# Kernel tuning notes

Measured on AMD Instinct MI355X. Metric: run time of the kernel, lower is better.

Reference implementation:

```python
import jax, jax.numpy as jnp
import numpy as np

B, C, H, W = 4, 3, 32, 32
N_IMAGES = 32
TIMESTEPS = 20


def _extract_patches(x, pad_mode):
    """3x3 patches at every spatial location. x: [B,C,H,W] -> [B,C,9,H,W]."""
    if pad_mode == 'wrap':
        xp = jnp.pad(x, ((0, 0), (0, 0), (1, 1), (1, 1)), mode='wrap')
    else:
        xp = jnp.pad(x, ((0, 0), (0, 0), (1, 1), (1, 1)))
    h, w = x.shape[2], x.shape[3]
    sl = [xp[:, :, di:di + h, dj:dj + w] for di in range(3) for dj in range(3)]
    return jnp.stack(sl, axis=2)  # [B,C,9,H,W], k = di*3+dj (torch unfold order)


def setup_inputs() -> dict:
    key = jax.random.key(0)
    k1, k2 = jax.random.split(key)
    x = jax.random.normal(k1, (B, C, H, W), dtype=jnp.float32)
    images = jax.random.uniform(k2, (N_IMAGES, C, H, W), dtype=jnp.float32)
    # linear beta schedule, as in _noise_buffers
    betas = jnp.linspace(1e-4, 0.02, TIMESTEPS, dtype=jnp.float32)
    alpha_cumprod = jnp.cumprod(1.0 - betas)
    mu_sched = jnp.sqrt(alpha_cumprod)
    sigma_sched = jnp.sqrt(1.0 - alpha_cumprod)
    return {"x": x, "images": images, "mu_sched": mu_sched,
            "sigma_sched": sigma_sched, "t": 10}


def reference(x, images, mu_sched, sigma_sched, t):
    mu = mu_sched[t]
    sigma = sigma_sched[t]
    b, c, h, w = x.shape

    # x-side: circular-padded 3x3 patches and their squared norms
    xp = _extract_patches(x, 'wrap').reshape(b, c * 9, h, w)   # [B,C*9,H,W]
    x_norms = jnp.sum(xp * xp, axis=1)                          # [B,H,W]

    # dataset-side: zero-padded 3x3 patches at every pixel of every image
    ip = _extract_patches(images, 'zeros')                      # [N,C,9,H,W]
    patches = ip.transpose(0, 3, 4, 1, 2).reshape(-1, c * 9)    # [P, C*9], P=N*H*W
    pnorms = jnp.sum(patches * patches, axis=1)                 # [P]
    pcenters = patches.reshape(-1, c, 9)[:, :, 4]               # [P,C] center pixel (1,1)

    # conv2d(x_pad, patches) == contraction over the C*9 patch axis
    conv = jnp.einsum('bkhw,pk->bphw', xp, patches)             # [B,P,H,W]

    inv2s2 = 1.0 / (2.0 * sigma * sigma)
    log_w = -(x_norms[:, None] - 2.0 * mu * conv
              + (mu * mu) * pnorms[None, :, None, None]) * inv2s2  # [B,P,H,W]

    # stable softmax-style weights over the patch axis (== online LSE result)
    m = jnp.max(log_w, axis=1)                                  # [B,H,W]
    wgt = jnp.exp(log_w - m[:, None])                           # [B,P,H,W]
    sum_w = jnp.sum(wgt, axis=1)                                # [B,H,W]

    # sum_p w * (x - mu * pcenter) = x*sum_w - mu * (w @ pcenters)
    wc = jnp.einsum('bphw,pc->bchw', wgt, pcenters)             # [B,C,H,W]
    sum_wd = x * sum_w[:, None] - mu * wc
    return -sum_wd / (sigma * sigma * sum_w[:, None])
```

## Files before the change

kernel.cpp:

```cpp
#include <hip/hip_runtime.h>
#include <cstddef>

#define P_TOTAL 32768
#define Q_TOTAL 4096
#define NSPLIT 128
#define KPS 256
#define TILES 16
#define NGROUP 8
#define QPERWG 256
#define NQG (Q_TOTAL / QPERWG)
#define GRID (NSPLIT * NQG)

#define KEYS_B 16384
#define VT_OFF KEYS_B
#define VT_PITCH 528
#define LDS_TOTAL (VT_OFF + 4 * VT_PITCH)

typedef _Float16 half8 __attribute__((ext_vector_type(8)));
typedef __fp16 fp16x2 __attribute__((ext_vector_type(2)));
typedef __fp16 fp16x4 __attribute__((ext_vector_type(4)));
typedef __fp16 fp16x8 __attribute__((ext_vector_type(8)));
typedef float floatx4 __attribute__((ext_vector_type(4)));

union h8cast { fp16x8 a; half8 b; };

__device__ __forceinline__ float fexp2(float x) {
#if defined(__has_builtin) && __has_builtin(__builtin_amdgcn_exp2f)
    return __builtin_amdgcn_exp2f(x);
#else
    return exp2f(x);
#endif
}

__global__ __launch_bounds__(256) void qbuild_k(
    const float* __restrict__ x, _Float16* __restrict__ q16)
{
    int q = blockIdx.x * 256 + threadIdx.x;
    int b = q >> 10, rem = q & 1023, h = rem >> 5, w = rem & 31;
    const float* xb = x + (size_t)b * 3072;
    _Float16 row[32];
    #pragma unroll
    for (int c = 0; c < 3; c++)
      #pragma unroll
      for (int di = 0; di < 3; di++)
        #pragma unroll
        for (int dj = 0; dj < 3; dj++)
            row[c * 9 + di * 3 + dj] =
                (_Float16)xb[c * 1024 + ((h + di + 31) & 31) * 32 + ((w + dj + 31) & 31)];
    row[27] = (_Float16)1.0f;
    row[28] = (_Float16)0.f; row[29] = (_Float16)0.f;
    row[30] = (_Float16)0.f; row[31] = (_Float16)0.f;
    _Float16* qp = q16 + (size_t)q * 32;
    #pragma unroll
    for (int u = 0; u < 4; u++) ((float4*)qp)[u] = ((float4*)row)[u];
}

__global__ __launch_bounds__(256) void score_k(
    const _Float16* __restrict__ q16, const float* __restrict__ images,
    const float* __restrict__ mu_sched, const float* __restrict__ sigma_sched,
    const int* __restrict__ tptr, float* __restrict__ partials)
{
    __shared__ char lds[LDS_TOTAL];
    int tid = threadIdx.x;
    int split = blockIdx.x >> 4;
    int qg    = blockIdx.x & 15;

    int t = tptr[0];
    float mu = mu_sched[t], sg = sigma_sched[t];
    const float LOG2E = 1.4426950408889634f;
    float inv2s2 = 1.0f / (2.0f * sg * sg);
    float s1     = 2.0f * mu * inv2s2 * LOG2E;
    float bscale = -mu * mu * inv2s2 * LOG2E;

    {
        int r = tid;
        int m16 = r & 15, tt = (r >> 4) & 1, tp = r >> 5;
        int kk = tp * 32 + (m16 >> 2) * 8 + tt * 4 + (m16 & 3);
        int p = split * KPS + kk;
        int n = p >> 10, rem = p & 1023, i = rem >> 5, j = rem & 31;
        const float* img = images + (size_t)n * 3072;
        _Float16 hrow[32];
        float pnorm = 0.f, c0 = 0.f, c1 = 0.f, c2 = 0.f;
        #pragma unroll
        for (int c = 0; c < 3; c++)
          #pragma unroll
          for (int di = 0; di < 3; di++)
            #pragma unroll
            for (int dj = 0; dj < 3; dj++) {
                int ii = i + di - 1, jj = j + dj - 1;
                float val = 0.f;
                if (ii >= 0 && ii < 32 && jj >= 0 && jj < 32)
                    val = img[c * 1024 + ii * 32 + jj];
                hrow[c * 9 + di * 3 + dj] = (_Float16)(val * s1);
                pnorm = fmaf(val, val, pnorm);
                if (di == 1 && dj == 1) { if (c == 0) c0 = val; else if (c == 1) c1 = val; else c2 = val; }
            }
        hrow[27] = (_Float16)(pnorm * bscale);
        hrow[28] = (_Float16)0.f; hrow[29] = (_Float16)0.f;
        hrow[30] = (_Float16)0.f; hrow[31] = (_Float16)0.f;
        int sw = (r >> 1) & 3;
        float4* src4 = (float4*)hrow;
        #pragma unroll
        for (int c = 0; c < 4; c++)
            *(float4*)(lds + r * 64 + ((c ^ sw) << 4)) = src4[c];
        _Float16* vt = (_Float16*)(lds + VT_OFF);
        vt[0 * (VT_PITCH / 2) + kk] = (_Float16)1.0f;
        vt[1 * (VT_PITCH / 2) + kk] = (_Float16)c0;
        vt[2 * (VT_PITCH / 2) + kk] = (_Float16)c1;
        vt[3 * (VT_PITCH / 2) + kk] = (_Float16)c2;
    }

    int lane = tid & 63, wid = tid >> 6;
    int col  = lane & 15, quad = lane >> 4;
    int qbase = qg * QPERWG + wid * 64;

    half8 qf[4];
    #pragma unroll
    for (int f = 0; f < 4; f++)
        qf[f] = *(const half8*)(q16 + (size_t)(qbase + f * 16 + col) * 32 + quad * 8);
    __syncthreads();

    int swc = (col >> 1) & 3;
    const char* abase = lds + col * 64 + ((quad ^ swc) << 4);

    float mx[4];
    {
        floatx4 mv[4];
        #pragma unroll
        for (int f = 0; f < 4; f++) mv[f] = (floatx4){-3e38f, -3e38f, -3e38f, -3e38f};
        #pragma unroll 4
        for (int tile = 0; tile < TILES; tile++) {
            half8 ak = *(const half8*)(abase + tile * 1024);
            #pragma unroll
            for (int f = 0; f < 4; f++) {
                floatx4 a = __builtin_amdgcn_mfma_f32_16x16x32_f16(
                    ak, qf[f], (floatx4){0.f, 0.f, 0.f, 0.f}, 0, 0, 0);
                mv[f] = __builtin_elementwise_max(mv[f], a);
            }
        }
        #pragma unroll
        for (int f = 0; f < 4; f++) {
            mx[f] = fmaxf(fmaxf(mv[f][0], mv[f][1]), fmaxf(mv[f][2], mv[f][3]));
            mx[f] = fmaxf(mx[f], __shfl_xor(mx[f], 16, 64));
            mx[f] = fmaxf(mx[f], __shfl_xor(mx[f], 32, 64));
        }
    }
    floatx4 nmv[4];
    #pragma unroll
    for (int f = 0; f < 4; f++)
        nmv[f] = (floatx4){-mx[f], -mx[f], -mx[f], -mx[f]};

    if (quad == 0) {
        #pragma unroll
        for (int f = 0; f < 4; f++)
            partials[(size_t)split * Q_TOTAL + qbase + f * 16 + col] = mx[f];
    }

    const char* vrow = lds + VT_OFF + col * VT_PITCH;
    floatx4 acc[4];
    #pragma unroll
    for (int f = 0; f < 4; f++) acc[f] = (floatx4){0.f, 0.f, 0.f, 0.f};

    #pragma unroll 2
    for (int g = 0; g < NGROUP; g++) {
        half8 ak0 = *(const half8*)(abase + (2 * g) * 1024);
        half8 ak1 = *(const half8*)(abase + (2 * g + 1) * 1024);
        half8 av = (half8)(_Float16)0.f;
        if (col < 4) av = *(const half8*)(vrow + g * 64 + quad * 16);
        #pragma unroll
        for (int f = 0; f < 4; f++) {
            floatx4 a0 = __builtin_amdgcn_mfma_f32_16x16x32_f16(ak0, qf[f], nmv[f], 0, 0, 0);
            floatx4 a1 = __builtin_amdgcn_mfma_f32_16x16x32_f16(ak1, qf[f], nmv[f], 0, 0, 0);
            fp16x2 p00 = __builtin_amdgcn_cvt_pkrtz(fexp2(a0[0]), fexp2(a0[1]));
            fp16x2 p01 = __builtin_amdgcn_cvt_pkrtz(fexp2(a0[2]), fexp2(a0[3]));
            fp16x2 p10 = __builtin_amdgcn_cvt_pkrtz(fexp2(a1[0]), fexp2(a1[1]));
            fp16x2 p11 = __builtin_amdgcn_cvt_pkrtz(fexp2(a1[2]), fexp2(a1[3]));
            fp16x4 lo = __builtin_shufflevector(p00, p01, 0, 1, 2, 3);
            fp16x4 hi = __builtin_shufflevector(p10, p11, 0, 1, 2, 3);
            h8cast u; u.a = __builtin_shufflevector(lo, hi, 0, 1, 2, 3, 4, 5, 6, 7);
            acc[f] = __builtin_amdgcn_mfma_f32_16x16x32_f16(av, u.b, acc[f], 0, 0, 0);
        }
    }

    if (quad == 0) {
        const size_t PL = (size_t)NSPLIT * Q_TOTAL;
        #pragma unroll
        for (int f = 0; f < 4; f++) {
            size_t idx = (size_t)split * Q_TOTAL + qbase + f * 16 + col;
            partials[idx + PL]     = acc[f][0];
            partials[idx + PL * 2] = acc[f][1];
            partials[idx + PL * 3] = acc[f][2];
            partials[idx + PL * 4] = acc[f][3];
        }
    }
}

__global__ __launch_bounds__(256) void combine_k(
    const float* __restrict__ x, const float* __restrict__ partials,
    const float* __restrict__ mu_sched, const float* __restrict__ sigma_sched,
    const int* __restrict__ tptr, float* __restrict__ out)
{
    int q = blockIdx.x * 256 + threadIdx.x;
    int t = tptr[0];
    float mu = mu_sched[t], sg = sigma_sched[t];
    float inv_s2 = 1.0f / (sg * sg);

    const size_t PL = (size_t)NSPLIT * Q_TOTAL;
    float M1 = -3e38f, S1 = 0.f, A1 = 0.f, B1 = 0.f, C1 = 0.f;
    float M2 = -3e38f, S2 = 0.f, A2 = 0.f, B2 = 0.f, C2 = 0.f;
    #pragma unroll 4
    for (int sp = 0; sp < NSPLIT / 2; sp++) {
        {
            size_t idx = (size_t)sp * Q_TOTAL + q;
            float mval = partials[idx];
            float mnew = fmaxf(M1, mval);
            float sco = fexp2(M1 - mnew), scn = fexp2(mval - mnew);
            S1 = fmaf(S1, sco, partials[idx + PL] * scn);
            A1 = fmaf(A1, sco, partials[idx + PL * 2] * scn);
            B1 = fmaf(B1, sco, partials[idx + PL * 3] * scn);
            C1 = fmaf(C1, sco, partials[idx + PL * 4] * scn);
            M1 = mnew;
        }
        {
            size_t idx = (size_t)(sp + NSPLIT / 2) * Q_TOTAL + q;
            float mval = partials[idx];
            float mnew = fmaxf(M2, mval);
            float sco = fexp2(M2 - mnew), scn = fexp2(mval - mnew);
            S2 = fmaf(S2, sco, partials[idx + PL] * scn);
            A2 = fmaf(A2, sco, partials[idx + PL * 2] * scn);
            B2 = fmaf(B2, sco, partials[idx + PL * 3] * scn);
            C2 = fmaf(C2, sco, partials[idx + PL * 4] * scn);
            M2 = mnew;
        }
    }
    float M = fmaxf(M1, M2);
    float r1 = fexp2(M1 - M), r2 = fexp2(M2 - M);
    float S  = S1 * r1 + S2 * r2;
    float W0 = A1 * r1 + A2 * r2;
    float W1 = B1 * r1 + B2 * r2;
    float W2 = C1 * r1 + C2 * r2;

    float invS = 1.0f / S;
    int b = q >> 10, rem = q & 1023;
    #pragma unroll
    for (int c = 0; c < 3; c++) {
        float Wc = (c == 0) ? W0 : (c == 1 ? W1 : W2);
        float xc = x[(size_t)b * 3072 + c * 1024 + rem];
        out[(size_t)b * 3072 + c * 1024 + rem] = -(xc - mu * Wc * invS) * inv_s2;
    }
}

extern "C" void kernel_launch(void* const* d_in, const int* in_sizes, int n_in,
                              void* d_out, int out_size, void* d_ws, size_t ws_size,
                              hipStream_t stream) {
    const float* x      = (const float*)d_in[0];
    const float* images = (const float*)d_in[1];
    const float* mu_s   = (const float*)d_in[2];
    const float* sg_s   = (const float*)d_in[3];
    const int*   tptr   = (const int*)d_in[4];
    float* out = (float*)d_out;

    float*    partials = (float*)d_ws;
    _Float16* q16      = (_Float16*)((char*)d_ws + (size_t)5 * NSPLIT * Q_TOTAL * 4);

    qbuild_k<<<Q_TOTAL / 256, 256, 0, stream>>>(x, q16);
    score_k<<<GRID, 256, 0, stream>>>(q16, images, mu_s, sg_s, tptr, partials);
    combine_k<<<Q_TOTAL / 256, 256, 0, stream>>>(
        x, partials, mu_s, sg_s, tptr, out);
}
```

Measured before the change: 110.9 us.

## Replace two-pass max/exp with online softmax, double splits, parallelize combine

The score kernel drops its separate max pass over all key tiles. It instead keeps a running max per query, rescaling the accumulator as each pair of tiles is processed, which halves the QK MFMA work. Keys per split are halved, so the grid doubles and each block builds only 128 keys (half the threads idle during the build). The combine kernel now splits the split axis across 4 waves and merges them through LDS, with 4x more blocks. The trade-offs are extra shuffle, rescale and exp work inside the loop, and twice as much partials traffic.

```diff
diff --git a/kernel.cpp b/kernel.cpp
--- a/kernel.cpp
+++ b/kernel.cpp
@@ -3,17 +3,16 @@
 
 #define P_TOTAL 32768
 #define Q_TOTAL 4096
-#define NSPLIT 128
-#define KPS 256
-#define TILES 16
-#define NGROUP 8
+#define NSPLIT 256
+#define KPS 128
+#define NGROUP 4
 #define QPERWG 256
 #define NQG (Q_TOTAL / QPERWG)
 #define GRID (NSPLIT * NQG)
 
-#define KEYS_B 16384
+#define KEYS_B (KPS * 64)
 #define VT_OFF KEYS_B
-#define VT_PITCH 528
+#define VT_PITCH 272
 #define LDS_TOTAL (VT_OFF + 4 * VT_PITCH)
 
 typedef _Float16 half8 __attribute__((ext_vector_type(8)));
@@ -72,7 +71,7 @@
     float s1     = 2.0f * mu * inv2s2 * LOG2E;
     float bscale = -mu * mu * inv2s2 * LOG2E;
 
-    {
+    if (tid < KPS) {
         int r = tid;
         int m16 = r & 15, tt = (r >> 4) & 1, tp = r >> 5;
         int kk = tp * 32 + (m16 >> 2) * 8 + tt * 4 + (m16 & 3);
@@ -122,46 +121,14 @@
 
     int swc = (col >> 1) & 3;
     const char* abase = lds + col * 64 + ((quad ^ swc) << 4);
-
-    float mx[4];
-    {
-        floatx4 mv[4];
-        #pragma unroll
-        for (int f = 0; f < 4; f++) mv[f] = (floatx4){-3e38f, -3e38f, -3e38f, -3e38f};
-        #pragma unroll 4
-        for (int tile = 0; tile < TILES; tile++) {
-            half8 ak = *(const half8*)(abase + tile * 1024);
-            #pragma unroll
-            for (int f = 0; f < 4; f++) {
-                floatx4 a = __builtin_amdgcn_mfma_f32_16x16x32_f16(
-                    ak, qf[f], (floatx4){0.f, 0.f, 0.f, 0.f}, 0, 0, 0);
-                mv[f] = __builtin_elementwise_max(mv[f], a);
-            }
-        }
-        #pragma unroll
-        for (int f = 0; f < 4; f++) {
-            mx[f] = fmaxf(fmaxf(mv[f][0], mv[f][1]), fmaxf(mv[f][2], mv[f][3]));
-            mx[f] = fmaxf(mx[f], __shfl_xor(mx[f], 16, 64));
-            mx[f] = fmaxf(mx[f], __shfl_xor(mx[f], 32, 64));
-        }
-    }
-    floatx4 nmv[4];
-    #pragma unroll
-    for (int f = 0; f < 4; f++)
-        nmv[f] = (floatx4){-mx[f], -mx[f], -mx[f], -mx[f]};
-
-    if (quad == 0) {
-        #pragma unroll
-        for (int f = 0; f < 4; f++)
-            partials[(size_t)split * Q_TOTAL + qbase + f * 16 + col] = mx[f];
-    }
-
-    const char* vrow = lds + VT_OFF + col * VT_PITCH;
+    const char* vrow  = lds + VT_OFF + col * VT_PITCH;
+
+    float mrun[4] = {-3e38f, -3e38f, -3e38f, -3e38f};
     floatx4 acc[4];
     #pragma unroll
     for (int f = 0; f < 4; f++) acc[f] = (floatx4){0.f, 0.f, 0.f, 0.f};
 
-    #pragma unroll 2
+    #pragma unroll
     for (int g = 0; g < NGROUP; g++) {
         half8 ak0 = *(const half8*)(abase + (2 * g) * 1024);
         half8 ak1 = *(const half8*)(abase + (2 * g + 1) * 1024);
@@ -169,12 +136,22 @@
         if (col < 4) av = *(const half8*)(vrow + g * 64 + quad * 16);
         #pragma unroll
         for (int f = 0; f < 4; f++) {
-            floatx4 a0 = __builtin_amdgcn_mfma_f32_16x16x32_f16(ak0, qf[f], nmv[f], 0, 0, 0);
-            floatx4 a1 = __builtin_amdgcn_mfma_f32_16x16x32_f16(ak1, qf[f], nmv[f], 0, 0, 0);
-            fp16x2 p00 = __builtin_amdgcn_cvt_pkrtz(fexp2(a0[0]), fexp2(a0[1]));
-            fp16x2 p01 = __builtin_amdgcn_cvt_pkrtz(fexp2(a0[2]), fexp2(a0[3]));
-            fp16x2 p10 = __builtin_amdgcn_cvt_pkrtz(fexp2(a1[0]), fexp2(a1[1]));
-            fp16x2 p11 = __builtin_amdgcn_cvt_pkrtz(fexp2(a1[2]), fexp2(a1[3]));
+            floatx4 a0 = __builtin_amdgcn_mfma_f32_16x16x32_f16(
+                ak0, qf[f], (floatx4){0.f, 0.f, 0.f, 0.f}, 0, 0, 0);
+            floatx4 a1 = __builtin_amdgcn_mfma_f32_16x16x32_f16(
+                ak1, qf[f], (floatx4){0.f, 0.f, 0.f, 0.f}, 0, 0, 0);
+            float L = fmaxf(fmaxf(fmaxf(a0[0], a0[1]), fmaxf(a0[2], a0[3])),
+                            fmaxf(fmaxf(a1[0], a1[1]), fmaxf(a1[2], a1[3])));
+            L = fmaxf(L, __shfl_xor(L, 16, 64));
+            L = fmaxf(L, __shfl_xor(L, 32, 64));
+            float mnew = fmaxf(mrun[f], L);
+            float scale = fexp2(mrun[f] - mnew);
+            mrun[f] = mnew;
+            acc[f] *= scale;
+            fp16x2 p00 = __builtin_amdgcn_cvt_pkrtz(fexp2(a0[0] - mnew), fexp2(a0[1] - mnew));
+            fp16x2 p01 = __builtin_amdgcn_cvt_pkrtz(fexp2(a0[2] - mnew), fexp2(a0[3] - mnew));
+            fp16x2 p10 = __builtin_amdgcn_cvt_pkrtz(fexp2(a1[0] - mnew), fexp2(a1[1] - mnew));
+            fp16x2 p11 = __builtin_amdgcn_cvt_pkrtz(fexp2(a1[2] - mnew), fexp2(a1[3] - mnew));
             fp16x4 lo = __builtin_shufflevector(p00, p01, 0, 1, 2, 3);
             fp16x4 hi = __builtin_shufflevector(p10, p11, 0, 1, 2, 3);
             h8cast u; u.a = __builtin_shufflevector(lo, hi, 0, 1, 2, 3, 4, 5, 6, 7);
@@ -187,6 +164,7 @@
         #pragma unroll
         for (int f = 0; f < 4; f++) {
             size_t idx = (size_t)split * Q_TOTAL + qbase + f * 16 + col;
+            partials[idx]          = mrun[f];
             partials[idx + PL]     = acc[f][0];
             partials[idx + PL * 2] = acc[f][1];
             partials[idx + PL * 3] = acc[f][2];
@@ -200,53 +178,54 @@
     const float* __restrict__ mu_sched, const float* __restrict__ sigma_sched,
     const int* __restrict__ tptr, float* __restrict__ out)
 {
-    int q = blockIdx.x * 256 + threadIdx.x;
+    __shared__ float red[5][4][64];
+    int tid = threadIdx.x;
+    int wid = tid >> 6, lane = tid & 63;
+    int q = blockIdx.x * 64 + lane;
     int t = tptr[0];
     float mu = mu_sched[t], sg = sigma_sched[t];
     float inv_s2 = 1.0f / (sg * sg);
 
     const size_t PL = (size_t)NSPLIT * Q_TOTAL;
-    float M1 = -3e38f, S1 = 0.f, A1 = 0.f, B1 = 0.f, C1 = 0.f;
-    float M2 = -3e38f, S2 = 0.f, A2 = 0.f, B2 = 0.f, C2 = 0.f;
+    float M = -3e38f, S = 0.f, W0 = 0.f, W1 = 0.f, W2 = 0.f;
+    int sp0 = wid * (NSPLIT / 4);
     #pragma unroll 4
-    for (int sp = 0; sp < NSPLIT / 2; sp++) {
-        {
-            size_t idx = (size_t)sp * Q_TOTAL + q;
-            float mval = partials[idx];
-            float mnew = fmaxf(M1, mval);
-            float sco = fexp2(M1 - mnew), scn = fexp2(mval - mnew);
-            S1 = fmaf(S1, sco, partials[idx + PL] * scn);
-            A1 = fmaf(A1, sco, partials[idx + PL * 2] * scn);
-            B1 = fmaf(B1, sco, partials[idx + PL * 3] * scn);
-            C1 = fmaf(C1, sco, partials[idx + PL * 4] * scn);
-            M1 = mnew;
-        }
-        {
-            size_t idx = (size_t)(sp + NSPLIT / 2) * Q_TOTAL + q;
-            float mval = partials[idx];
-            float mnew = fmaxf(M2, mval);
-            float sco = fexp2(M2 - mnew), scn = fexp2(mval - mnew);
-            S2 = fmaf(S2, sco, partials[idx + PL] * scn);
-            A2 = fmaf(A2, sco, partials[idx + PL * 2] * scn);
-            B2 = fmaf(B2, sco, partials[idx + PL * 3] * scn);
-            C2 = fmaf(C2, sco, partials[idx + PL * 4] * scn);
-            M2 = mnew;
-        }
-    }
-    float M = fmaxf(M1, M2);
-    float r1 = fexp2(M1 - M), r2 = fexp2(M2 - M);
-    float S  = S1 * r1 + S2 * r2;
-    float W0 = A1 * r1 + A2 * r2;
-    float W1 = B1 * r1 + B2 * r2;
-    float W2 = C1 * r1 + C2 * r2;
-
-    float invS = 1.0f / S;
-    int b = q >> 10, rem = q & 1023;
-    #pragma unroll
-    for (int c = 0; c < 3; c++) {
-        float Wc = (c == 0) ? W0 : (c == 1 ? W1 : W2);
-        float xc = x[(size_t)b * 3072 + c * 1024 + rem];
-        out[(size_t)b * 3072 + c * 1024 + rem] = -(xc - mu * Wc * invS) * inv_s2;
+    for (int i = 0; i < NSPLIT / 4; i++) {
+        size_t idx = (size_t)(sp0 + i) * Q_TOTAL + q;
+        float mval = partials[idx];
+        float mnew = fmaxf(M, mval);
+        float sco = fexp2(M - mnew), scn = fexp2(mval - mnew);
+        S  = fmaf(S,  sco, partials[idx + PL] * scn);
+        W0 = fmaf(W0, sco, partials[idx + PL * 2] * scn);
+        W1 = fmaf(W1, sco, partials[idx + PL * 3] * scn);
+        W2 = fmaf(W2, sco, partials[idx + PL * 4] * scn);
+        M = mnew;
+    }
+    red[0][wid][lane] = M;  red[1][wid][lane] = S;
+    red[2][wid][lane] = W0; red[3][wid][lane] = W1; red[4][wid][lane] = W2;
+    __syncthreads();
+
+    if (wid == 0) {
+        float Mf = red[0][0][lane];
+        #pragma unroll
+        for (int wv = 1; wv < 4; wv++) Mf = fmaxf(Mf, red[0][wv][lane]);
+        float Sf = 0.f, A = 0.f, B = 0.f, C = 0.f;
+        #pragma unroll
+        for (int wv = 0; wv < 4; wv++) {
+            float r = fexp2(red[0][wv][lane] - Mf);
+            Sf = fmaf(red[1][wv][lane], r, Sf);
+            A  = fmaf(red[2][wv][lane], r, A);
+            B  = fmaf(red[3][wv][lane], r, B);
+            C  = fmaf(red[4][wv][lane], r, C);
+        }
+        float invS = 1.0f / Sf;
+        int b = q >> 10, rem = q & 1023;
+        #pragma unroll
+        for (int c = 0; c < 3; c++) {
+            float Wc = (c == 0) ? A : (c == 1 ? B : C);
+            float xc = x[(size_t)b * 3072 + c * 1024 + rem];
+            out[(size_t)b * 3072 + c * 1024 + rem] = -(xc - mu * Wc * invS) * inv_s2;
+        }
     }
 }
 
@@ -265,6 +244,6 @@
 
     qbuild_k<<<Q_TOTAL / 256, 256, 0, stream>>>(x, q16);
     score_k<<<GRID, 256, 0, stream>>>(q16, images, mu_s, sg_s, tptr, partials);
-    combine_k<<<Q_TOTAL / 256, 256, 0, stream>>>(
+    combine_k<<<Q_TOTAL / 64, 256, 0, stream>>>(
         x, partials, mu_s, sg_s, tptr, out);
 }
```

Measured after the change: 113.5 us. 1.02x slower.
